# Kernel optimization log

Hardware: AMD Instinct MI355X
Metric: run time of the kernel (lower is better)

## Reference

```python
import jax, jax.numpy as jnp
import numpy as np

B, T, C, H, L, E, K, V = 4, 1024, 1024, 16, 2, 8, 2, 32000
HD = C // H
CAP = B * T * K // E  # expert capacity with capacity_factor=1.0 -> 2048


def setup_inputs() -> dict:
    key = jax.random.key(0)
    ks = iter(jax.random.split(key, 16))
    def rn(shape, s=0.02):
        return jax.random.normal(next(ks), shape, jnp.float32) * s
    return {
        'input_ids': jax.random.randint(next(ks), (B, T), 0, V),
        'noise': jax.random.normal(next(ks), (L, B, T, E), jnp.float32),
        'tok_emb': rn((V, C)),
        'pos_emb': rn((T, C)),
        'ln1_w': jnp.ones((L, C)), 'ln1_b': jnp.zeros((L, C)),
        'qkv_w': rn((L, 3 * C, C)), 'out_w': rn((L, C, C)),
        'ln2_w': jnp.ones((L, C)), 'ln2_b': jnp.zeros((L, C)),
        'rt_w': rn((L, E, C)), 'rt_b': jnp.zeros((L, E)),
        'nz_w': rn((L, E, C)), 'nz_b': jnp.zeros((L, E)),
        'e_w1': rn((L, E, 4 * C, C)), 'e_b1': jnp.zeros((L, E, 4 * C)),
        'e_w2': rn((L, E, C, 4 * C)), 'e_b2': jnp.zeros((L, E, C)),
        'lnf_w': jnp.ones((C,)), 'lnf_b': jnp.zeros((C,)),
        'head_w': rn((1, C)), 'head_b': jnp.zeros((1,)),
    }


def _ln(x, w, b):
    m = jnp.mean(x, -1, keepdims=True)
    v = jnp.mean(jnp.square(x - m), -1, keepdims=True)
    return (x - m) * jax.lax.rsqrt(v + 1e-5) * w + b


def _attn(x, qkv_w, out_w):
    # non-causal flash-attention equivalent (softmax_scale = 1/sqrt(head_size))
    qkv = (x @ qkv_w.T).reshape(B, T, 3, H, HD)
    q, k, v = qkv[:, :, 0], qkv[:, :, 1], qkv[:, :, 2]
    s = jnp.einsum('bthd,bshd->bhts', q, k) / np.float32(np.sqrt(HD))
    p = jax.nn.softmax(s, axis=-1)
    o = jnp.einsum('bhts,bshd->bthd', p, v).reshape(B, T, C)
    return o @ out_w.T


def _moe(x, rt_w, rt_b, nz_w, nz_b, w1, b1, w2, b2, noise):
    logits = x @ rt_w.T + rt_b                      # [B,T,E]
    noise_logits = x @ nz_w.T + nz_b
    noisy = logits + noise * jax.nn.softplus(noise_logits)
    topv, topi = jax.lax.top_k(noisy, K)            # [B,T,K]
    gates = jax.nn.softmax(topv, axis=-1)           # softmax over sparse (-inf filled) logits == softmax over top-k
    oh = jax.nn.one_hot(topi, E, dtype=x.dtype)     # [B,T,K,E]
    router = jnp.einsum('btk,btke->bte', gates, oh)
    N = B * T
    flat_x = x.reshape(N, C)
    flat_r = router.reshape(N, E)
    flat_i = topi.reshape(N, K)
    updates = jnp.zeros_like(flat_x)
    for i in range(E):  # per-expert gather -> FFN -> scatter, capacity-limited in token order
        mask = jnp.any(flat_i == i, axis=-1)        # [N]
        pos = jnp.cumsum(mask) - 1
        keep = mask & (pos < CAP)
        sel = jnp.argsort(jnp.logical_not(keep))[:CAP]  # stable: kept tokens first, original order
        valid = keep[sel].astype(x.dtype)
        xi = flat_x[sel]                             # [CAP,C]
        h = jax.nn.relu(xi @ w1[i].T + b1[i])
        out = h @ w2[i].T + b2[i]
        gate = flat_r[sel, i] * valid
        updates = updates.at[sel].add(out * gate[:, None])
    return updates.reshape(B, T, C)


def reference(input_ids, noise, tok_emb, pos_emb, ln1_w, ln1_b, qkv_w, out_w,
              ln2_w, ln2_b, rt_w, rt_b, nz_w, nz_b, e_w1, e_b1, e_w2, e_b2,
              lnf_w, lnf_b, head_w, head_b):
    x = tok_emb[input_ids] + pos_emb[None, :T]
    for l in range(L):
        x = x + _attn(_ln(x, ln1_w[l], ln1_b[l]), qkv_w[l], out_w[l])
        x = x + _moe(_ln(x, ln2_w[l], ln2_b[l]), rt_w[l], rt_b[l], nz_w[l], nz_b[l],
                     e_w1[l], e_b1[l], e_w2[l], e_b2[l], noise[l])
    x = _ln(x, lnf_w, lnf_b)
    return jnp.mean(x, axis=1) @ head_w.T + head_b  # [B,1]
```

## Files before the change

kernel.cpp:

```cpp
#include <hip/hip_runtime.h>
#include <hip/hip_bf16.h>
#include <math.h>

namespace {

constexpr int B = 4, T = 1024, C = 1024, Hh = 16, L = 2, E = 8, HD = 64;
constexpr int NTOK = B * T;
constexpr int CAP = 1024;
constexpr int C3 = 3 * C, C4 = 4 * C;

typedef __attribute__((ext_vector_type(8))) short bf16x8;
typedef __attribute__((ext_vector_type(8))) short short8;
typedef __attribute__((ext_vector_type(4))) float f32x4;

static __device__ __forceinline__ short f2b(float f) {
  __hip_bfloat16 h = __float2bfloat16(f);
  return *reinterpret_cast<short*>(&h);
}
static __device__ __forceinline__ float b2f(unsigned short u) {
  union { unsigned int i; float f; } v; v.i = (unsigned int)u << 16; return v.f;
}

#define SWZ(row, kb) (((row) << 7) + ((kb) ^ (((row) & 7) << 4)))

static __device__ __forceinline__ void gload16(const void* g, void* l) {
  __builtin_amdgcn_global_load_lds((const __attribute__((address_space(1))) void*)g,
                                   (__attribute__((address_space(3))) void*)l, 16, 0, 0);
}

__global__ __launch_bounds__(256) void cvt4_kernel(
    const float* __restrict__ s0, const float* __restrict__ s1,
    const float* __restrict__ s2, const float* __restrict__ s3,
    unsigned short* __restrict__ d0, unsigned short* __restrict__ d1,
    unsigned short* __restrict__ d2, unsigned short* __restrict__ d3) {
  constexpr size_t N0 = (size_t)L * C3 * C, N1 = (size_t)L * C * C;
  constexpr size_t N2 = (size_t)L * E * C4 * C;
  size_t i = ((size_t)blockIdx.x * 256 + threadIdx.x) * 8;
  const float* s; unsigned short* d; size_t off;
  if (i < N0)                { s = s0; d = d0; off = i; }
  else if (i < N0 + N1)      { s = s1; d = d1; off = i - N0; }
  else if (i < N0 + N1 + N2) { s = s2; d = d2; off = i - N0 - N1; }
  else                       { s = s3; d = d3; off = i - N0 - N1 - N2; }
  float4 v0 = *(const float4*)(s + off);
  float4 v1 = *(const float4*)(s + off + 4);
  short8 r;
  r[0] = f2b(v0.x); r[1] = f2b(v0.y); r[2] = f2b(v0.z); r[3] = f2b(v0.w);
  r[4] = f2b(v1.x); r[5] = f2b(v1.y); r[6] = f2b(v1.z); r[7] = f2b(v1.w);
  *(short8*)(d + off) = r;
}

__global__ __launch_bounds__(256) void embed_kernel(const int* __restrict__ ids,
    const float* __restrict__ tok, const float* __restrict__ pos, float* __restrict__ x) {
  int idx = blockIdx.x * 256 + threadIdx.x;
  int n = idx >> 8;
  int c4 = idx & 255;
  int t = n & (T - 1);
  int id = ids[n];
  float4 a = ((const float4*)(tok + (size_t)id * C))[c4];
  float4 p = ((const float4*)(pos + (size_t)t * C))[c4];
  float4 r{a.x + p.x, a.y + p.y, a.z + p.z, a.w + p.w};
  ((float4*)x)[idx] = r;
}

__global__ __launch_bounds__(256) void ln_kernel(const float* __restrict__ in,
    const unsigned short* __restrict__ eo, const int* __restrict__ slot0,
    const int* __restrict__ slot1, float* __restrict__ xupd,
    float* __restrict__ out, unsigned short* __restrict__ outb,
    const float* __restrict__ w, const float* __restrict__ b) {
  constexpr size_t SLICE = (size_t)E * CAP * C;
  __shared__ float red[8];
  int row = blockIdx.x, tid = threadIdx.x;
  float4 v = ((const float4*)(in + (size_t)row * C))[tid];
  if (eo) {
    int s0 = slot0[row], s1 = slot1[row];
    auto addslot = [&](int s) {
      if (s < 0) return;
      const unsigned short* p0 = eo + (size_t)s * C + tid * 4;
      short4 u = *(const short4*)p0;
      short4 u2 = *(const short4*)(p0 + SLICE);
      v.x += b2f((unsigned short)u.x) + b2f((unsigned short)u2.x);
      v.y += b2f((unsigned short)u.y) + b2f((unsigned short)u2.y);
      v.z += b2f((unsigned short)u.z) + b2f((unsigned short)u2.z);
      v.w += b2f((unsigned short)u.w) + b2f((unsigned short)u2.w);
    };
    addslot(s0);
    addslot(s1);
    if (xupd) ((float4*)(xupd + (size_t)row * C))[tid] = v;
  }
  float s = v.x + v.y + v.z + v.w;
  #pragma unroll
  for (int off = 32; off > 0; off >>= 1) s += __shfl_down(s, off);
  if ((tid & 63) == 0) red[tid >> 6] = s;
  __syncthreads();
  float mean = (red[0] + red[1] + red[2] + red[3]) * (1.f / C);
  __syncthreads();
  float dx = v.x - mean, dy = v.y - mean, dz = v.z - mean, dw = v.w - mean;
  float sq = dx * dx + dy * dy + dz * dz + dw * dw;
  #pragma unroll
  for (int off = 32; off > 0; off >>= 1) sq += __shfl_down(sq, off);
  if ((tid & 63) == 0) red[tid >> 6] = sq;
  __syncthreads();
  float var = (red[0] + red[1] + red[2] + red[3]) * (1.f / C);
  float rs = rsqrtf(var + 1e-5f);
  float4 wc = ((const float4*)w)[tid];
  float4 bc = ((const float4*)b)[tid];
  float4 o{dx * rs * wc.x + bc.x, dy * rs * wc.y + bc.y,
           dz * rs * wc.z + bc.z, dw * rs * wc.w + bc.w};
  if (out) ((float4*)(out + (size_t)row * C))[tid] = o;
  if (outb) {
    short4 ob{f2b(o.x), f2b(o.y), f2b(o.z), f2b(o.w)};
    *(short4*)(outb + (size_t)row * C + tid * 4) = ob;
  }
}

template<bool GATHER, bool RELU, bool BIAS, bool XCDMAP, int OUTMODE, int SPLITK>
__global__ __launch_bounds__(512, 2) void gemm8p(
    const unsigned short* __restrict__ A, const unsigned short* __restrict__ W,
    const float* __restrict__ bias, unsigned short* __restrict__ Cout,
    const int* __restrict__ rowidx, const float* __restrict__ rowscale,
    const int* __restrict__ cnts, int M, int N, int Kd,
    size_t strideA, size_t strideW, size_t strideOut, int strideBias, int GY)
{
  __shared__ alignas(16) char smem[131072];
  int bx, by, e, ksl;
  if constexpr (XCDMAP) {
    int fid = blockIdx.x; e = fid & 7; int r1 = fid >> 3;
    ksl = r1 & (SPLITK - 1); int wi = r1 / SPLITK;
    by = wi % GY; bx = wi / GY;
  } else { bx = blockIdx.x; by = blockIdx.y; e = 0; ksl = 0; }
  int Mr = M;
  if (cnts) { int cc = cnts[e]; Mr = cc < M ? cc : M; }
  int row0 = by * 256, col0 = bx * 256;
  if (row0 >= Mr) return;

  const int kLen = Kd / SPLITK;
  const unsigned short* Ap = A + (size_t)e * strideA;
  const unsigned short* Wp = W + (size_t)e * strideW;
  const int* ridx = rowidx ? rowidx + (size_t)e * CAP : nullptr;

  int t = threadIdx.x;
  int l = t & 63, lm = l & 15, lg = l >> 4;
  int w = t >> 6, wm = w >> 2, wn = w & 3;

  const char* srcA[2];
  const char* srcB[2];
  #pragma unroll
  for (int j = 0; j < 2; j++) {
    int flat = t + j * 512;
    int row = flat >> 2;
    int c16 = (flat & 3) ^ ((row >> 1) & 3);
    int ga;
    if constexpr (GATHER) {
      int ar = row0 + row; if (ar >= Mr) ar = Mr - 1; ga = ridx[ar];
    } else ga = row0 + row;
    srcA[j] = (const char*)Ap + (size_t)ga * Kd * 2 + (size_t)ksl * kLen * 2 + c16 * 16;
    srcB[j] = (const char*)Wp + (size_t)(col0 + row) * Kd * 2 + (size_t)ksl * kLen * 2 + c16 * 16;
  }
  int dst0 = t * 16, dst1 = t * 16 + 8192;

  auto STAGE = [&](int buf, int op, int kh, int kt) {
    size_t goff = (size_t)kt * 128 + kh * 64;
    char* base = smem + buf * 65536 + op * 32768 + kh * 16384;
    if (op) {
      gload16(srcB[0] + goff, base + dst0);
      gload16(srcB[1] + goff, base + dst1);
    } else {
      gload16(srcA[0] + goff, base + dst0);
      gload16(srcA[1] + goff, base + dst1);
    }
  };

  int colswz = (lg ^ ((lm >> 1) & 3)) * 16;

  f32x4 acc[8][4];
  #pragma unroll
  for (int i = 0; i < 8; i++)
    #pragma unroll
    for (int j = 0; j < 4; j++) acc[i][j] = f32x4{0.f, 0.f, 0.f, 0.f};

  STAGE(0, 0, 0, 0); STAGE(0, 1, 0, 0); STAGE(0, 0, 1, 0); STAGE(0, 1, 1, 0);
  asm volatile("s_waitcnt vmcnt(0)" ::: "memory");
  __builtin_amdgcn_s_barrier();

  int NT = kLen >> 6;
  bf16x8 bfr[4];
  for (int k = 0; k < NT; k++) {
    int cur = k & 1, nxt = cur ^ 1;
    bool pf = (k + 1 < NT);
    #pragma unroll
    for (int ph = 0; ph < 4; ph++) {
      const int ks = ph >> 1, mh = ph & 1;
      bf16x8 afr[4];
      #pragma unroll
      for (int i = 0; i < 4; i++) {
        int row = wm * 128 + (mh * 4 + i) * 16 + lm;
        afr[i] = *(const bf16x8*)(smem + cur * 65536 + ks * 16384 + row * 64 + colswz);
      }
      if (mh == 0) {
        #pragma unroll
        for (int i = 0; i < 4; i++) {
          int row = wn * 64 + i * 16 + lm;
          bfr[i] = *(const bf16x8*)(smem + cur * 65536 + 32768 + ks * 16384 + row * 64 + colswz);
        }
      }
      if (pf) STAGE(nxt, mh, ks, k + 1);
      if (mh == 1) {
        if (pf) asm volatile("s_waitcnt vmcnt(4)" ::: "memory");
        else    asm volatile("s_waitcnt vmcnt(0)" ::: "memory");
      }
      __builtin_amdgcn_s_barrier();
      __builtin_amdgcn_s_setprio(1);
      #pragma unroll
      for (int i = 0; i < 4; i++)
        #pragma unroll
        for (int ni = 0; ni < 4; ni++)
          acc[mh * 4 + i][ni] =
              __builtin_amdgcn_mfma_f32_16x16x32_bf16(afr[i], bfr[ni], acc[mh * 4 + i][ni], 0, 0, 0);
      __builtin_amdgcn_s_setprio(0);
      __builtin_amdgcn_s_barrier();
    }
  }

  float cbias[4];
  #pragma unroll
  for (int ni = 0; ni < 4; ni++)
    cbias[ni] = (BIAS && ksl == 0) ? bias[(size_t)e * strideBias + col0 + wn * 64 + ni * 16 + lm] : 0.f;

  #pragma unroll
  for (int mi = 0; mi < 8; mi++) {
    #pragma unroll
    for (int rr = 0; rr < 4; rr++) {
      int m = row0 + wm * 128 + mi * 16 + lg * 4 + rr;
      if (m >= Mr) continue;
      if constexpr (OUTMODE == 0) {
        unsigned short* cp = Cout + (size_t)e * strideOut + (size_t)m * N + col0 + wn * 64 + lm;
        #pragma unroll
        for (int ni = 0; ni < 4; ni++) {
          float v = acc[mi][ni][rr] + cbias[ni];
          if constexpr (RELU) v = fmaxf(v, 0.f);
          cp[ni * 16] = (unsigned short)f2b(v);
        }
      } else {
        float sc = rowscale[(size_t)e * CAP + m];
        unsigned short* cp = Cout + (size_t)ksl * ((size_t)E * CAP * N)
                             + ((size_t)e * CAP + m) * N + col0 + wn * 64 + lm;
        #pragma unroll
        for (int ni = 0; ni < 4; ni++) {
          float v = acc[mi][ni][rr] + cbias[ni];
          cp[ni * 16] = (unsigned short)f2b(sc * v);
        }
      }
    }
  }
}

__global__ __launch_bounds__(256) void gemm_proj(
    const unsigned short* __restrict__ A, const unsigned short* __restrict__ W,
    float* __restrict__ Cout, int M, int N, int Kd)
{
  int bx = blockIdx.x, by = blockIdx.y;
  int row0 = by * 128, col0 = bx * 128;

  __shared__ alignas(16) char smem[32768];
  char* Ab = smem;
  char* Bb = smem + 16384;

  int t = threadIdx.x, w = t >> 6, l = t & 63;
  int lm = l & 15, lg = l >> 4;
  int wr = w >> 1, wc = w & 1;

  int lrow8 = l >> 3;
  int scol = ((l & 7) ^ lrow8) << 4;
  const char* srcA[4];
  const char* srcB[4];
  #pragma unroll
  for (int i = 0; i < 4; i++) {
    int seg = w * 4 + i;
    int rloc = seg * 8 + lrow8;
    srcA[i] = (const char*)A + (size_t)(row0 + rloc) * Kd * 2 + scol;
    srcB[i] = (const char*)W + (size_t)(col0 + rloc) * Kd * 2 + scol;
  }

  f32x4 acc[4][4];
  #pragma unroll
  for (int i = 0; i < 4; i++)
    #pragma unroll
    for (int j = 0; j < 4; j++) acc[i][j] = f32x4{0.f, 0.f, 0.f, 0.f};

  int NT = Kd >> 6;
  for (int kt = 0; kt < NT; kt++) {
    __syncthreads();
    #pragma unroll
    for (int i = 0; i < 4; i++) {
      int seg = w * 4 + i;
      gload16(srcA[i], Ab + seg * 1024);
      gload16(srcB[i], Bb + seg * 1024);
      srcA[i] += 128;
      srcB[i] += 128;
    }
    __syncthreads();
    #pragma unroll
    for (int ks = 0; ks < 2; ks++) {
      bf16x8 af[4], bfr[4];
      #pragma unroll
      for (int mi = 0; mi < 4; mi++)
        af[mi] = *(const bf16x8*)(Ab + SWZ(wr * 64 + mi * 16 + lm, ks * 64 + lg * 16));
      #pragma unroll
      for (int ni = 0; ni < 4; ni++)
        bfr[ni] = *(const bf16x8*)(Bb + SWZ(wc * 64 + ni * 16 + lm, ks * 64 + lg * 16));
      #pragma unroll
      for (int mi = 0; mi < 4; mi++)
        #pragma unroll
        for (int ni = 0; ni < 4; ni++)
          acc[mi][ni] = __builtin_amdgcn_mfma_f32_16x16x32_bf16(af[mi], bfr[ni], acc[mi][ni], 0, 0, 0);
    }
  }

  #pragma unroll
  for (int mi = 0; mi < 4; mi++) {
    #pragma unroll
    for (int rr = 0; rr < 4; rr++) {
      int m = row0 + wr * 64 + mi * 16 + lg * 4 + rr;
      float* cp = Cout + (size_t)m * N + col0 + wc * 64 + lm;
      #pragma unroll
      for (int ni = 0; ni < 4; ni++) cp[ni * 16] += acc[mi][ni][rr];
    }
  }
}

__global__ __launch_bounds__(256) void attn_mfma(const unsigned short* __restrict__ qkv,
                                                 unsigned short* __restrict__ ao) {
  __shared__ alignas(16) char smem[20480];
  char* Ks = smem;
  char* Vt = smem + 4096;
  char* Pb = smem + 12288;

  int t = threadIdx.x, w = t >> 6, lane = t & 63, lm = lane & 15, lg = lane >> 4;
  int qt = blockIdx.x, bh = blockIdx.y, b = bh >> 4, h = bh & 15;
  const unsigned short* base = qkv + (size_t)b * T * C3;

  bf16x8 qf[2];
  {
    int qrow = qt * 64 + w * 16 + lm;
    const unsigned short* qp = base + (size_t)qrow * C3 + h * HD + lg * 8;
    qf[0] = *(const bf16x8*)qp;
    qf[1] = *(const bf16x8*)(qp + 32);
  }

  f32x4 o[4];
  #pragma unroll
  for (int i = 0; i < 4; i++) o[i] = f32x4{0.f, 0.f, 0.f, 0.f};
  float mrun[4] = {-INFINITY, -INFINITY, -INFINITY, -INFINITY};
  float lpart[4] = {0.f, 0.f, 0.f, 0.f};

  int ksrow = t >> 3, kc = (t & 7) * 8;
  int vdl = t & 7;
  bf16x8 kreg;
  unsigned short vv[8];
  auto LOADKV = [&](int s0) {
    kreg = *(const bf16x8*)(base + (size_t)(s0 + ksrow) * C3 + C + h * HD + kc);
    const unsigned short* vp = base + (size_t)(s0 + ksrow) * C3 + 2 * C + h * HD + vdl;
    #pragma unroll
    for (int i = 0; i < 8; i++) vv[i] = vp[8 * i];
  };

  LOADKV(0);
  for (int s0 = 0; s0 < T; s0 += 32) {
    __syncthreads();
    *(bf16x8*)(Ks + SWZ(ksrow, kc * 2)) = kreg;
    #pragma unroll
    for (int i = 0; i < 8; i++) {
      int d = 8 * i + vdl;
      *(short*)(Vt + (d << 7) + ((ksrow * 2) ^ ((d & 7) << 4))) = (short)vv[i];
    }
    __syncthreads();
    if (s0 + 32 < T) LOADKV(s0 + 32);

    f32x4 sacc[2];
    sacc[0] = f32x4{0.f, 0.f, 0.f, 0.f};
    sacc[1] = f32x4{0.f, 0.f, 0.f, 0.f};
    #pragma unroll
    for (int ni = 0; ni < 2; ni++)
      #pragma unroll
      for (int ks = 0; ks < 2; ks++) {
        bf16x8 kfrag = *(const bf16x8*)(Ks + SWZ(ni * 16 + lm, ks * 64 + lg * 16));
        sacc[ni] = __builtin_amdgcn_mfma_f32_16x16x32_bf16(qf[ks], kfrag, sacc[ni], 0, 0, 0);
      }

    float sv0[4], sv1[4], pv[8];
    bool okd = true;
    #pragma unroll
    for (int r = 0; r < 4; r++) {
      sv0[r] = sacc[0][r] * 0.125f;
      sv1[r] = sacc[1][r] * 0.125f;
      okd = okd && (fmaxf(sv0[r], sv1[r]) <= mrun[r] + 8.f);
    }
    if (__all(okd ? 1 : 0)) {
      #pragma unroll
      for (int r = 0; r < 4; r++) {
        float p0 = __expf(sv0[r] - mrun[r]);
        float p1 = __expf(sv1[r] - mrun[r]);
        lpart[r] += p0 + p1;
        pv[r] = p0; pv[4 + r] = p1;
      }
    } else {
      float fr[4];
      #pragma unroll
      for (int r = 0; r < 4; r++) {
        float tmax = fmaxf(sv0[r], sv1[r]);
        #pragma unroll
        for (int mk = 1; mk < 16; mk <<= 1) tmax = fmaxf(tmax, __shfl_xor(tmax, mk));
        float mn = fmaxf(mrun[r], tmax);
        float f = __expf(mrun[r] - mn);
        float p0 = __expf(sv0[r] - mn), p1 = __expf(sv1[r] - mn);
        lpart[r] = lpart[r] * f + p0 + p1;
        mrun[r] = mn;
        fr[r] = f;
        pv[r] = p0; pv[4 + r] = p1;
      }
      #pragma unroll
      for (int ni = 0; ni < 4; ni++) {
        o[ni][0] *= fr[0]; o[ni][1] *= fr[1]; o[ni][2] *= fr[2]; o[ni][3] *= fr[3];
      }
    }

    char* P = Pb + w * 2048;
    #pragma unroll
    for (int ni = 0; ni < 2; ni++)
      #pragma unroll
      for (int r = 0; r < 4; r++) {
        int q = lg * 4 + r;
        int kbyte = (ni * 16 + lm) * 2;
        *(short*)(P + (q << 7) + (kbyte ^ ((q & 7) << 4))) = f2b(pv[ni * 4 + r]);
      }
    bf16x8 pfrag = *(const bf16x8*)(P + SWZ(lm, lg * 16));
    #pragma unroll
    for (int ni = 0; ni < 4; ni++) {
      bf16x8 vfrag = *(const bf16x8*)(Vt + SWZ(ni * 16 + lm, lg * 16));
      o[ni] = __builtin_amdgcn_mfma_f32_16x16x32_bf16(pfrag, vfrag, o[ni], 0, 0, 0);
    }
  }

  float inv[4];
  #pragma unroll
  for (int r = 0; r < 4; r++) {
    float lsum = lpart[r];
    #pragma unroll
    for (int mk = 1; mk < 16; mk <<= 1) lsum += __shfl_xor(lsum, mk);
    inv[r] = 1.f / lsum;
  }
  #pragma unroll
  for (int r = 0; r < 4; r++) {
    int qrow = qt * 64 + w * 16 + lg * 4 + r;
    unsigned short* dst = ao + (size_t)(b * T + qrow) * C + h * HD + lm;
    #pragma unroll
    for (int ni = 0; ni < 4; ni++) dst[ni * 16] = (unsigned short)f2b(o[ni][r] * inv[r]);
  }
}

__global__ __launch_bounds__(64) void router_kernel(
    const float* __restrict__ xin, const float* __restrict__ rt_w, const float* __restrict__ rt_b,
    const float* __restrict__ nz_w, const float* __restrict__ nz_b, const float* __restrict__ noise,
    int* __restrict__ i0, int* __restrict__ i1, float* __restrict__ g0, float* __restrict__ g1,
    int* __restrict__ slot0, int* __restrict__ slot1)
{
  int n = blockIdx.x, lane = threadIdx.x;
  const float* xr = xin + (size_t)n * C;
  float acc[16];
  #pragma unroll
  for (int e = 0; e < 16; e++) acc[e] = 0.f;
  for (int c = lane; c < C; c += 64) {
    float xv = xr[c];
    #pragma unroll
    for (int e = 0; e < 8; e++) {
      acc[e]     += xv * rt_w[e * C + c];
      acc[8 + e] += xv * nz_w[e * C + c];
    }
  }
  #pragma unroll
  for (int e = 0; e < 16; e++) {
    #pragma unroll
    for (int off = 32; off > 0; off >>= 1) acc[e] += __shfl_down(acc[e], off);
  }
  if (lane == 0) {
    float nv[8];
    #pragma unroll
    for (int e = 0; e < 8; e++) {
      float lgt = acc[e] + rt_b[e];
      float nl = acc[8 + e] + nz_b[e];
      float sp = fmaxf(nl, 0.f) + log1pf(expf(-fabsf(nl)));
      nv[e] = lgt + noise[(size_t)n * E + e] * sp;
    }
    float v0 = -INFINITY, v1 = -INFINITY; int b0 = -1, b1 = -1;
    #pragma unroll
    for (int e = 0; e < 8; e++) {
      float v = nv[e];
      if (v > v0)      { v1 = v0; b1 = b0; v0 = v; b0 = e; }
      else if (v > v1) { v1 = v; b1 = e; }
    }
    float ex = expf(v1 - v0);
    float inv = 1.f / (1.f + ex);
    i0[n] = b0; i1[n] = b1;
    g0[n] = inv; g1[n] = ex * inv;
    slot0[n] = -1; slot1[n] = -1;
  }
}

__global__ __launch_bounds__(512) void capacity_kernel(
    const int* __restrict__ i0, const int* __restrict__ i1,
    const float* __restrict__ g0, const float* __restrict__ g1,
    int* __restrict__ sel, float* __restrict__ gsel, int* __restrict__ counts,
    int* __restrict__ slot0, int* __restrict__ slot1)
{
  int e = threadIdx.x >> 6, lane = threadIdx.x & 63;
  int cnt = 0;
  unsigned long long ltmask = (lane == 0) ? 0ull : (~0ull >> (64 - lane));
  int a = i0[lane], bb = i1[lane];
  for (int basei = 0; basei < NTOK; basei += 64) {
    int na = 0, nb = 0;
    if (basei + 64 < NTOK) { na = i0[basei + 64 + lane]; nb = i1[basei + 64 + lane]; }
    int tt = basei + lane;
    bool match = (a == e) || (bb == e);
    unsigned long long mk = __ballot(match);
    int pos = cnt + __popcll(mk & ltmask);
    if (match && pos < CAP) {
      sel[e * CAP + pos] = tt;
      gsel[e * CAP + pos] = (a == e) ? g0[tt] : g1[tt];
      if (a == e) slot0[tt] = e * CAP + pos;
      else        slot1[tt] = e * CAP + pos;
    }
    cnt += __popcll(mk);
    a = na; bb = nb;
  }
  if (lane == 0) counts[e] = cnt < CAP ? cnt : CAP;
}

__global__ __launch_bounds__(256) void head_kernel(const float* __restrict__ xin,
    const float* __restrict__ hw, const float* __restrict__ hb, float* __restrict__ out)
{
  __shared__ float red[8];
  int b = blockIdx.x, tid = threadIdx.x;
  float4 wv = ((const float4*)hw)[tid];
  float s = 0.f;
  for (int t = 0; t < T; t++) {
    float4 v = ((const float4*)(xin + (size_t)(b * T + t) * C))[tid];
    s += v.x * wv.x + v.y * wv.y + v.z * wv.z + v.w * wv.w;
  }
  #pragma unroll
  for (int off = 32; off > 0; off >>= 1) s += __shfl_down(s, off);
  if ((tid & 63) == 0) red[tid >> 6] = s;
  __syncthreads();
  if (tid == 0) out[b] = (red[0] + red[1] + red[2] + red[3]) * (1.f / T) + hb[0];
}

}

extern "C" void kernel_launch(void* const* d_in, const int* in_sizes, int n_in,
                              void* d_out, int out_size, void* d_ws, size_t ws_size,
                              hipStream_t stream) {
  (void)in_sizes; (void)n_in; (void)out_size; (void)ws_size;
  const int*   ids     = (const int*)d_in[0];
  const float* noise   = (const float*)d_in[1];
  const float* tok_emb = (const float*)d_in[2];
  const float* pos_emb = (const float*)d_in[3];
  const float* ln1_w   = (const float*)d_in[4];
  const float* ln1_b   = (const float*)d_in[5];
  const float* qkv_w   = (const float*)d_in[6];
  const float* out_w   = (const float*)d_in[7];
  const float* ln2_w   = (const float*)d_in[8];
  const float* ln2_b   = (const float*)d_in[9];
  const float* rt_w    = (const float*)d_in[10];
  const float* rt_b    = (const float*)d_in[11];
  const float* nz_w    = (const float*)d_in[12];
  const float* nz_b    = (const float*)d_in[13];
  const float* e_w1    = (const float*)d_in[14];
  const float* e_b1    = (const float*)d_in[15];
  const float* e_w2    = (const float*)d_in[16];
  const float* e_b2    = (const float*)d_in[17];
  const float* lnf_w   = (const float*)d_in[18];
  const float* lnf_b   = (const float*)d_in[19];
  const float* head_w  = (const float*)d_in[20];
  const float* head_b  = (const float*)d_in[21];
  float* out = (float*)d_out;

  char* wsp = (char*)d_ws;
  size_t off = 0;
  auto alloc = [&](size_t n) { char* p = wsp + off; off += (n + 255) & ~(size_t)255; return p; };
  float* x    = (float*)alloc((size_t)NTOK * C * 4);
  float* t1   = (float*)alloc((size_t)NTOK * C * 4);
  unsigned short* t1b  = (unsigned short*)alloc((size_t)NTOK * C * 2);
  unsigned short* qkvb = (unsigned short*)alloc((size_t)NTOK * C3 * 2);
  unsigned short* aob  = (unsigned short*)alloc((size_t)NTOK * C * 2);
  unsigned short* hbuf = (unsigned short*)alloc((size_t)E * CAP * C4 * 2);
  unsigned short* eo   = (unsigned short*)alloc((size_t)2 * E * CAP * C * 2);
  unsigned short* qkvw_b = (unsigned short*)alloc((size_t)L * C3 * C * 2);
  unsigned short* outw_b = (unsigned short*)alloc((size_t)L * C * C * 2);
  unsigned short* ew1_b  = (unsigned short*)alloc((size_t)L * E * C4 * C * 2);
  unsigned short* ew2_b  = (unsigned short*)alloc((size_t)L * E * C * C4 * 2);
  int*   i0   = (int*)alloc(NTOK * 4);
  int*   i1   = (int*)alloc(NTOK * 4);
  float* g0   = (float*)alloc(NTOK * 4);
  float* g1   = (float*)alloc(NTOK * 4);
  int*   sel  = (int*)alloc(E * CAP * 4);
  float* gsel = (float*)alloc(E * CAP * 4);
  int*   counts = (int*)alloc(E * 4);
  int*   slot0  = (int*)alloc(NTOK * 4);
  int*   slot1  = (int*)alloc(NTOK * 4);

  {
    constexpr size_t TOT = (size_t)L * C3 * C + (size_t)L * C * C + 2 * (size_t)L * E * C4 * C;
    cvt4_kernel<<<(int)(TOT / 2048), 256, 0, stream>>>(qkv_w, out_w, e_w1, e_w2,
                                                       qkvw_b, outw_b, ew1_b, ew2_b);
  }

  embed_kernel<<<NTOK * C / 4 / 256, 256, 0, stream>>>(ids, tok_emb, pos_emb, x);

  for (int l = 0; l < L; l++) {
    if (l == 0)
      ln_kernel<<<NTOK, 256, 0, stream>>>(x, nullptr, nullptr, nullptr, nullptr,
                                          nullptr, t1b, ln1_w + l * C, ln1_b + l * C);
    else
      ln_kernel<<<NTOK, 256, 0, stream>>>(x, eo, slot0, slot1, x,
                                          nullptr, t1b, ln1_w + l * C, ln1_b + l * C);
    gemm8p<false, false, false, false, 0, 1><<<dim3(C3 / 256, NTOK / 256), 512, 0, stream>>>(
        t1b, qkvw_b + (size_t)l * C3 * C, nullptr, qkvb,
        nullptr, nullptr, nullptr, NTOK, C3, C, 0, 0, 0, 0, 0);
    attn_mfma<<<dim3(T / 64, B * Hh), 256, 0, stream>>>(qkvb, aob);
    gemm_proj<<<dim3(C / 128, NTOK / 128), 256, 0, stream>>>(
        aob, outw_b + (size_t)l * C * C, x, NTOK, C, C);

    ln_kernel<<<NTOK, 256, 0, stream>>>(x, nullptr, nullptr, nullptr, nullptr,
                                        t1, t1b, ln2_w + l * C, ln2_b + l * C);
    router_kernel<<<NTOK, 64, 0, stream>>>(t1, rt_w + (size_t)l * E * C, rt_b + l * E,
        nz_w + (size_t)l * E * C, nz_b + l * E, noise + (size_t)l * NTOK * E,
        i0, i1, g0, g1, slot0, slot1);
    capacity_kernel<<<1, 512, 0, stream>>>(i0, i1, g0, g1, sel, gsel, counts, slot0, slot1);

    gemm8p<true, true, true, true, 0, 1><<<(C4 / 256) * (CAP / 256) * E, 512, 0, stream>>>(
        t1b, ew1_b + (size_t)l * E * C4 * C, e_b1 + (size_t)l * E * C4, hbuf,
        sel, nullptr, counts, CAP, C4, C,
        0, (size_t)C4 * C, (size_t)CAP * C4, C4, CAP / 256);
    gemm8p<false, false, true, true, 2, 2><<<(C / 256) * (CAP / 256) * 2 * E, 512, 0, stream>>>(
        hbuf, ew2_b + (size_t)l * E * C * C4, e_b2 + (size_t)l * E * C, eo,
        nullptr, gsel, counts, CAP, C, C4,
        (size_t)CAP * C4, (size_t)C * C4, 0, C, CAP / 256);
  }

  ln_kernel<<<NTOK, 256, 0, stream>>>(x, eo, slot0, slot1, nullptr,
                                      t1, nullptr, lnf_w, lnf_b);
  head_kernel<<<B, 256, 0, stream>>>(t1, head_w, head_b, out);
}
```

Baseline: 899.1 us.

## Fuse fp32-to-bf16 weight conversion into GEMM B-operand loads

Removes the separate pre-pass that converted the QKV and expert weights to bf16. The GEMM now loads fp32 weights directly into registers, packs them to bf16 and writes them to swizzled LDS, avoiding a full read-write pass over the large weight set. The cost is that each weight tile is now read at fp32 width, and tiles are reread by every row block. The pipeline also changes: B goes through registers instead of direct-to-LDS loads, and a full vmcnt/lgkmcnt wait replaces the partial wait, which may reduce the overlap of loads with compute.

```diff
diff --git a/kernel.cpp b/kernel.cpp
--- a/kernel.cpp
+++ b/kernel.cpp
@@ -20,6 +20,12 @@
 static __device__ __forceinline__ float b2f(unsigned short u) {
   union { unsigned int i; float f; } v; v.i = (unsigned int)u << 16; return v.f;
 }
+static __device__ __forceinline__ bf16x8 pack8(float4 a, float4 b) {
+  bf16x8 r;
+  r[0] = f2b(a.x); r[1] = f2b(a.y); r[2] = f2b(a.z); r[3] = f2b(a.w);
+  r[4] = f2b(b.x); r[5] = f2b(b.y); r[6] = f2b(b.z); r[7] = f2b(b.w);
+  return r;
+}
 
 #define SWZ(row, kb) (((row) << 7) + ((kb) ^ (((row) & 7) << 4)))
 
@@ -28,25 +34,15 @@
                                    (__attribute__((address_space(3))) void*)l, 16, 0, 0);
 }
 
-__global__ __launch_bounds__(256) void cvt4_kernel(
-    const float* __restrict__ s0, const float* __restrict__ s1,
-    const float* __restrict__ s2, const float* __restrict__ s3,
-    unsigned short* __restrict__ d0, unsigned short* __restrict__ d1,
-    unsigned short* __restrict__ d2, unsigned short* __restrict__ d3) {
-  constexpr size_t N0 = (size_t)L * C3 * C, N1 = (size_t)L * C * C;
-  constexpr size_t N2 = (size_t)L * E * C4 * C;
+__global__ __launch_bounds__(256) void cvt_kernel(const float* __restrict__ in,
+    unsigned short* __restrict__ out) {
   size_t i = ((size_t)blockIdx.x * 256 + threadIdx.x) * 8;
-  const float* s; unsigned short* d; size_t off;
-  if (i < N0)                { s = s0; d = d0; off = i; }
-  else if (i < N0 + N1)      { s = s1; d = d1; off = i - N0; }
-  else if (i < N0 + N1 + N2) { s = s2; d = d2; off = i - N0 - N1; }
-  else                       { s = s3; d = d3; off = i - N0 - N1 - N2; }
-  float4 v0 = *(const float4*)(s + off);
-  float4 v1 = *(const float4*)(s + off + 4);
+  float4 v0 = *(const float4*)(in + i);
+  float4 v1 = *(const float4*)(in + i + 4);
   short8 r;
   r[0] = f2b(v0.x); r[1] = f2b(v0.y); r[2] = f2b(v0.z); r[3] = f2b(v0.w);
   r[4] = f2b(v1.x); r[5] = f2b(v1.y); r[6] = f2b(v1.z); r[7] = f2b(v1.w);
-  *(short8*)(d + off) = r;
+  *(short8*)(out + i) = r;
 }
 
 __global__ __launch_bounds__(256) void embed_kernel(const int* __restrict__ ids,
@@ -115,7 +111,7 @@
 
 template<bool GATHER, bool RELU, bool BIAS, bool XCDMAP, int OUTMODE, int SPLITK>
 __global__ __launch_bounds__(512, 2) void gemm8p(
-    const unsigned short* __restrict__ A, const unsigned short* __restrict__ W,
+    const unsigned short* __restrict__ A, const float* __restrict__ W,
     const float* __restrict__ bias, unsigned short* __restrict__ Cout,
     const int* __restrict__ rowidx, const float* __restrict__ rowscale,
     const int* __restrict__ cnts, int M, int N, int Kd,
@@ -135,7 +131,7 @@
 
   const int kLen = Kd / SPLITK;
   const unsigned short* Ap = A + (size_t)e * strideA;
-  const unsigned short* Wp = W + (size_t)e * strideW;
+  const float* Wp = W + (size_t)e * strideW;
   const int* ridx = rowidx ? rowidx + (size_t)e * CAP : nullptr;
 
   int t = threadIdx.x;
@@ -143,7 +139,6 @@
   int w = t >> 6, wm = w >> 2, wn = w & 3;
 
   const char* srcA[2];
-  const char* srcB[2];
   #pragma unroll
   for (int j = 0; j < 2; j++) {
     int flat = t + j * 512;
@@ -154,22 +149,41 @@
       int ar = row0 + row; if (ar >= Mr) ar = Mr - 1; ga = ridx[ar];
     } else ga = row0 + row;
     srcA[j] = (const char*)Ap + (size_t)ga * Kd * 2 + (size_t)ksl * kLen * 2 + c16 * 16;
-    srcB[j] = (const char*)Wp + (size_t)(col0 + row) * Kd * 2 + (size_t)ksl * kLen * 2 + c16 * 16;
   }
   int dst0 = t * 16, dst1 = t * 16 + 8192;
 
-  auto STAGE = [&](int buf, int op, int kh, int kt) {
+  auto STAGEA = [&](int buf, int kh, int kt) {
     size_t goff = (size_t)kt * 128 + kh * 64;
-    char* base = smem + buf * 65536 + op * 32768 + kh * 16384;
-    if (op) {
-      gload16(srcB[0] + goff, base + dst0);
-      gload16(srcB[1] + goff, base + dst1);
-    } else {
-      gload16(srcA[0] + goff, base + dst0);
-      gload16(srcA[1] + goff, base + dst1);
-    }
+    char* base = smem + buf * 65536 + kh * 16384;
+    gload16(srcA[0] + goff, base + dst0);
+    gload16(srcA[1] + goff, base + dst1);
   };
 
+  int brow = t & 255;
+  int bc16 = (t >> 8) * 2;
+  const float* bsrc = Wp + (size_t)(col0 + brow) * Kd + (size_t)ksl * kLen;
+  float4 breg[8];
+  auto LOADB = [&](int kt) {
+    const float* p = bsrc + kt * 64;
+    #pragma unroll
+    for (int kh = 0; kh < 2; kh++)
+      #pragma unroll
+      for (int j = 0; j < 2; j++) {
+        breg[kh * 4 + j * 2]     = *(const float4*)(p + kh * 32 + (bc16 + j) * 8);
+        breg[kh * 4 + j * 2 + 1] = *(const float4*)(p + kh * 32 + (bc16 + j) * 8 + 4);
+      }
+  };
+  auto WRITEB = [&](int buf) {
+    #pragma unroll
+    for (int kh = 0; kh < 2; kh++)
+      #pragma unroll
+      for (int j = 0; j < 2; j++) {
+        int c16s = (bc16 + j) ^ ((brow >> 1) & 3);
+        *(bf16x8*)(smem + buf * 65536 + 32768 + kh * 16384 + brow * 64 + c16s * 16)
+            = pack8(breg[kh * 4 + j * 2], breg[kh * 4 + j * 2 + 1]);
+      }
+  };
+
   int colswz = (lg ^ ((lm >> 1) & 3)) * 16;
 
   f32x4 acc[8][4];
@@ -178,8 +192,11 @@
     #pragma unroll
     for (int j = 0; j < 4; j++) acc[i][j] = f32x4{0.f, 0.f, 0.f, 0.f};
 
-  STAGE(0, 0, 0, 0); STAGE(0, 1, 0, 0); STAGE(0, 0, 1, 0); STAGE(0, 1, 1, 0);
+  LOADB(0);
+  STAGEA(0, 0, 0); STAGEA(0, 1, 0);
+  WRITEB(0);
   asm volatile("s_waitcnt vmcnt(0)" ::: "memory");
+  asm volatile("s_waitcnt lgkmcnt(0)" ::: "memory");
   __builtin_amdgcn_s_barrier();
 
   int NT = kLen >> 6;
@@ -203,10 +220,12 @@
           bfr[i] = *(const bf16x8*)(smem + cur * 65536 + 32768 + ks * 16384 + row * 64 + colswz);
         }
       }
-      if (pf) STAGE(nxt, mh, ks, k + 1);
-      if (mh == 1) {
-        if (pf) asm volatile("s_waitcnt vmcnt(4)" ::: "memory");
-        else    asm volatile("s_waitcnt vmcnt(0)" ::: "memory");
+      if (ph == 0 && pf) LOADB(k + 1);
+      if (ph == 1 && pf) { STAGEA(nxt, 0, k + 1); STAGEA(nxt, 1, k + 1); }
+      if (ph == 3) {
+        if (pf) WRITEB(nxt);
+        asm volatile("s_waitcnt vmcnt(0)" ::: "memory");
+        asm volatile("s_waitcnt lgkmcnt(0)" ::: "memory");
       }
       __builtin_amdgcn_s_barrier();
       __builtin_amdgcn_s_setprio(1);
@@ -593,10 +612,7 @@
   unsigned short* aob  = (unsigned short*)alloc((size_t)NTOK * C * 2);
   unsigned short* hbuf = (unsigned short*)alloc((size_t)E * CAP * C4 * 2);
   unsigned short* eo   = (unsigned short*)alloc((size_t)2 * E * CAP * C * 2);
-  unsigned short* qkvw_b = (unsigned short*)alloc((size_t)L * C3 * C * 2);
   unsigned short* outw_b = (unsigned short*)alloc((size_t)L * C * C * 2);
-  unsigned short* ew1_b  = (unsigned short*)alloc((size_t)L * E * C4 * C * 2);
-  unsigned short* ew2_b  = (unsigned short*)alloc((size_t)L * E * C * C4 * 2);
   int*   i0   = (int*)alloc(NTOK * 4);
   int*   i1   = (int*)alloc(NTOK * 4);
   float* g0   = (float*)alloc(NTOK * 4);
@@ -607,11 +623,7 @@
   int*   slot0  = (int*)alloc(NTOK * 4);
   int*   slot1  = (int*)alloc(NTOK * 4);
 
-  {
-    constexpr size_t TOT = (size_t)L * C3 * C + (size_t)L * C * C + 2 * (size_t)L * E * C4 * C;
-    cvt4_kernel<<<(int)(TOT / 2048), 256, 0, stream>>>(qkv_w, out_w, e_w1, e_w2,
-                                                       qkvw_b, outw_b, ew1_b, ew2_b);
-  }
+  cvt_kernel<<<(int)((size_t)L * C * C / 2048), 256, 0, stream>>>(out_w, outw_b);
 
   embed_kernel<<<NTOK * C / 4 / 256, 256, 0, stream>>>(ids, tok_emb, pos_emb, x);
 
@@ -623,7 +635,7 @@
       ln_kernel<<<NTOK, 256, 0, stream>>>(x, eo, slot0, slot1, x,
                                           nullptr, t1b, ln1_w + l * C, ln1_b + l * C);
     gemm8p<false, false, false, false, 0, 1><<<dim3(C3 / 256, NTOK / 256), 512, 0, stream>>>(
-        t1b, qkvw_b + (size_t)l * C3 * C, nullptr, qkvb,
+        t1b, qkv_w + (size_t)l * C3 * C, nullptr, qkvb,
         nullptr, nullptr, nullptr, NTOK, C3, C, 0, 0, 0, 0, 0);
     attn_mfma<<<dim3(T / 64, B * Hh), 256, 0, stream>>>(qkvb, aob);
     gemm_proj<<<dim3(C / 128, NTOK / 128), 256, 0, stream>>>(
@@ -637,11 +649,11 @@
     capacity_kernel<<<1, 512, 0, stream>>>(i0, i1, g0, g1, sel, gsel, counts, slot0, slot1);
 
     gemm8p<true, true, true, true, 0, 1><<<(C4 / 256) * (CAP / 256) * E, 512, 0, stream>>>(
-        t1b, ew1_b + (size_t)l * E * C4 * C, e_b1 + (size_t)l * E * C4, hbuf,
+        t1b, e_w1 + (size_t)l * E * C4 * C, e_b1 + (size_t)l * E * C4, hbuf,
         sel, nullptr, counts, CAP, C4, C,
         0, (size_t)C4 * C, (size_t)CAP * C4, C4, CAP / 256);
     gemm8p<false, false, true, true, 2, 2><<<(C / 256) * (CAP / 256) * 2 * E, 512, 0, stream>>>(
-        hbuf, ew2_b + (size_t)l * E * C * C4, e_b2 + (size_t)l * E * C, eo,
+        hbuf, e_w2 + (size_t)l * E * C * C4, e_b2 + (size_t)l * E * C, eo,
         nullptr, gsel, counts, CAP, C, C4,
         (size_t)CAP * C4, (size_t)C * C4, 0, C, CAP / 256);
   }
```

Result: slower. 1.067 ms (+18.7%).
